# Kernel optimization log

Hardware: AMD Instinct MI355X
Metric: run time of the kernel (lower is better)

## Reference

```python
import jax, jax.numpy as jnp
import numpy as np

B, N, H, BIN, E = 16, 100, 300, 11, 20000


def setup_inputs() -> dict:
    key = jax.random.key(0)
    k1, k2, k3, k4, k5 = jax.random.split(key, 5)
    local_feats = jax.random.normal(k1, (B, N, H), dtype=jnp.float32)
    binary_feats = jax.random.normal(k2, (B, N, N, BIN), dtype=jnp.float32)
    sparse_idx = jax.random.randint(k3, (E, 3), 0, B).astype(jnp.int64)
    W1 = jax.random.normal(k4, (H + BIN, H), dtype=jnp.float32) * 0.02
    b1 = jnp.zeros((H,), dtype=jnp.float32)
    W2 = jax.random.normal(k5, (H, 1), dtype=jnp.float32) * 0.02
    b2 = jnp.zeros((1,), dtype=jnp.float32)
    return {"local_feats": local_feats, "binary_feats": binary_feats,
            "sparse_idx": sparse_idx, "W1": W1, "b1": b1, "W2": W2, "b2": b2}


def reference(local_feats, binary_feats, sparse_idx, W1, b1, W2, b2):
    # local_pair[b,i,j] = local_feats[b,j] + local_feats[b,i]  -> [B,N,N,H]
    local_pair = local_feats[:, None, :, :] + local_feats[:, :, None, :]
    all_feats = jnp.concatenate([local_pair, binary_feats], axis=-1)  # [B,N,N,H+BIN]
    att = jax.nn.relu(jnp.einsum('bijk,kh->bijh', all_feats, W1) + b1)  # [B,N,N,H]
    score = jax.nn.sigmoid(jnp.einsum('bijh,ho->bijo', att, W2) + b2)   # [B,N,N,1]
    # weighted sum over dim j (torch dim=2 of [B,1,N,H]*[B,N,N,1])
    global_feats = jnp.sum(local_feats[:, None, :, :] * score, axis=2)  # [B,N,H]
    bb, ii, jj = sparse_idx[:, 0], sparse_idx[:, 1], sparse_idx[:, 2]
    global_pair = global_feats[bb, ii] + global_feats[bb, jj]  # [E,H]
    local_pair_g = local_pair[bb, ii, jj]                      # [E,H]
    return (local_pair_g, global_pair)
```

## Files before the change

### kernel.cpp

```cpp
#include <hip/hip_runtime.h>

#define BB 16
#define NN 100
#define HH 300
#define EE 20000

typedef __bf16 bf16x8 __attribute__((ext_vector_type(8)));
typedef float f32x4 __attribute__((ext_vector_type(4)));

__device__ __forceinline__ unsigned short f2bf_u(float v) {
  const unsigned u = __builtin_bit_cast(unsigned, v);
  return (unsigned short)((u + 0x7FFFu + ((u >> 16) & 1u)) >> 16);
}
__device__ __forceinline__ __bf16 f2bf(float v) {
  unsigned short s = f2bf_u(v);
  return __builtin_bit_cast(__bf16, s);
}

#define OFF_GF 0
#define OFF_U 307200

__global__ __launch_bounds__(256) void k_projD(
    const float* __restrict__ X, const float* __restrict__ W1,
    const float* __restrict__ b1, const int* __restrict__ sp,
    float* __restrict__ out, float* __restrict__ U) {
  const int bid = (int)blockIdx.x;
  const int tid = (int)threadIdx.x;

  if (bid < 475) {
    const int wave = tid >> 6;
    const int lane = tid & 63;
    const int tile = bid * 4 + wave;
    const int mt = tile / 19;
    const int nt = tile - mt * 19;
    const int r0 = mt * 16;
    const int n0 = nt * 16;
    const int l15 = lane & 15;
    const int lk = (lane >> 4) * 8;

    bf16x8 xa[10];
    {
      const float* __restrict__ xr = X + (size_t)(r0 + l15) * 300;
#pragma unroll
      for (int kc = 0; kc < 10; ++kc) {
        const int k0 = lk + kc * 32;
        if (k0 + 7 < 300) {
          const float4 a = *reinterpret_cast<const float4*>(xr + k0);
          const float4 c = *reinterpret_cast<const float4*>(xr + k0 + 4);
          xa[kc][0] = f2bf(a.x); xa[kc][1] = f2bf(a.y);
          xa[kc][2] = f2bf(a.z); xa[kc][3] = f2bf(a.w);
          xa[kc][4] = f2bf(c.x); xa[kc][5] = f2bf(c.y);
          xa[kc][6] = f2bf(c.z); xa[kc][7] = f2bf(c.w);
        } else {
#pragma unroll
          for (int t = 0; t < 8; ++t) {
            const int k = k0 + t;
            xa[kc][t] = f2bf((k < 300) ? xr[k] : 0.f);
          }
        }
      }
    }
    bf16x8 wb[10];
    {
      const int col = n0 + l15;
      const bool cok = (col < 300);
#pragma unroll
      for (int kc = 0; kc < 10; ++kc) {
#pragma unroll
        for (int t = 0; t < 8; ++t) {
          const int k = lk + kc * 32 + t;
          const float v = (cok && k < 300) ? W1[(size_t)k * 300 + col] : 0.f;
          wb[kc][t] = f2bf(v);
        }
      }
    }

    f32x4 acc = {0.f, 0.f, 0.f, 0.f};
#pragma unroll
    for (int kc = 0; kc < 10; ++kc)
      acc = __builtin_amdgcn_mfma_f32_16x16x32_bf16(xa[kc], wb[kc], acc, 0, 0, 0);

    const int h = n0 + l15;
    if (h < 300) {
      const float hb = 0.5f * b1[h];
      const int rbase = r0 + (lane >> 4) * 4;
#pragma unroll
      for (int reg = 0; reg < 4; ++reg)
        U[(size_t)(rbase + reg) * 300 + h] = acc[reg] + hb;
    }
  } else {
    const float4* __restrict__ X4 = (const float4*)X;
    float4* __restrict__ out0 = (float4*)out;
    const int nb = (int)gridDim.x - 475;
    for (int idx = (bid - 475) * 256 + tid; idx < EE * 75; idx += nb * 256) {
      const int e = idx / 75;
      const int c = idx - e * 75;
      const int b = sp[e * 3 + 0];
      const int ii = sp[e * 3 + 1];
      const int jj = sp[e * 3 + 2];
      const float4 xi = X4[(b * 100 + ii) * 75 + c];
      const float4 xj = X4[(b * 100 + jj) * 75 + c];
      out0[idx] =
          make_float4(xi.x + xj.x, xi.y + xj.y, xi.z + xj.z, xi.w + xj.w);
    }
  }
}

__global__ __launch_bounds__(1024) void k_scoreGF3(
    const float* __restrict__ X, const float* __restrict__ U,
    const float* __restrict__ W1, const float* __restrict__ W2,
    const float* __restrict__ b2, const float* __restrict__ Bin,
    float* __restrict__ gf) {
  __shared__ float s_bin[1100];
  __shared__ float s_part[7][2][16];
  __shared__ float s_score[100];
  __shared__ float s_gpart[4][300];
  __shared__ __align__(16) unsigned short s_w1bt[304 * 40];

  const int bi = (int)blockIdx.x;
  const int b = bi >> 4;
  const int i = bi & 15;
  const int tid = (int)threadIdx.x;
  const int wv = tid >> 6;
  const int jt = wv >> 1;
  const int nth = wv & 1;
  const int lane = tid & 63;
  const int l15 = lane & 15;
  const int lk = (lane >> 4) * 8;

  for (int t = tid; t < 1100; t += 1024)
    s_bin[t] = Bin[(size_t)(b * 100 + i) * 1100 + t];
  for (int e = tid; e < 304 * 40; e += 1024) {
    const int row = e / 40;
    const int k = e - row * 40;
    float v = 0.f;
    if (k < 11 && row < 300) v = W1[(size_t)(300 + k) * 300 + row];
    s_w1bt[e] = f2bf_u(v);
  }
  __syncthreads();

  if (jt < 7) {
    bf16x8 af;
    const int jrl = jt * 16 + l15;
    const int jr_cl = (jrl < 100) ? jrl : 99;
#pragma unroll
    for (int t = 0; t < 8; ++t) {
      const int k = lk + t;
      af[t] = (k < 11) ? f2bf(s_bin[jr_cl * 11 + k]) : f2bf(0.f);
    }

    const int jbase = jt * 16 + (lane >> 4) * 4;
    int jrow[4];
#pragma unroll
    for (int reg = 0; reg < 4; ++reg)
      jrow[reg] = (jbase + reg < 100) ? (jbase + reg) : 99;

    const float* __restrict__ Ui = U + (size_t)(b * 100 + i) * 300;
    float jacc[4] = {0.f, 0.f, 0.f, 0.f};

    auto step = [&](int nt) {
      const bf16x8 bf = *reinterpret_cast<const bf16x8*>(
          &s_w1bt[(nt * 16 + l15) * 40 + lk]);
      const int h = nt * 16 + l15;
      const int hc = (h < 300) ? h : 299;
      const float ui = Ui[hc];
      const float w2v = (h < 300) ? W2[h] : 0.f;
      f32x4 cin;
#pragma unroll
      for (int reg = 0; reg < 4; ++reg)
        cin[reg] = ui + U[(size_t)(b * 100 + jrow[reg]) * 300 + hc];
      const f32x4 d =
          __builtin_amdgcn_mfma_f32_16x16x32_bf16(af, bf, cin, 0, 0, 0);
#pragma unroll
      for (int reg = 0; reg < 4; ++reg)
        jacc[reg] = fmaf(fmaxf(d[reg], 0.f), w2v, jacc[reg]);
    };
    if (nth == 0) {
#pragma unroll
      for (int t = 0; t < 10; ++t) step(t);
    } else {
#pragma unroll
      for (int t = 0; t < 9; ++t) step(10 + t);
    }

#pragma unroll
    for (int reg = 0; reg < 4; ++reg) {
      float p = jacc[reg];
#pragma unroll
      for (int m = 8; m >= 1; m >>= 1) p += __shfl_xor(p, m, 64);
      if (l15 == 0) s_part[jt][nth][(lane >> 4) * 4 + reg] = p;
    }
  }
  __syncthreads();

  if (tid < 100) {
    const float p = s_part[tid >> 4][0][tid & 15] +
                    s_part[tid >> 4][1][tid & 15] + b2[0];
    s_score[tid] = 1.f / (1.f + __expf(-p));
  }
  __syncthreads();

  for (int item = tid; item < 1200; item += 1024) {
    const int jq = item / 300;
    const int col = item - jq * 300;
    const float* __restrict__ Xr = X + (size_t)(b * 100 + jq * 25) * 300 + col;
    float g0 = 0.f, g1 = 0.f, g2 = 0.f, g3 = 0.f, g4 = 0.f;
#pragma unroll
    for (int jl = 0; jl < 25; jl += 5) {
      g0 = fmaf(Xr[(jl + 0) * 300], s_score[jq * 25 + jl + 0], g0);
      g1 = fmaf(Xr[(jl + 1) * 300], s_score[jq * 25 + jl + 1], g1);
      g2 = fmaf(Xr[(jl + 2) * 300], s_score[jq * 25 + jl + 2], g2);
      g3 = fmaf(Xr[(jl + 3) * 300], s_score[jq * 25 + jl + 3], g3);
      g4 = fmaf(Xr[(jl + 4) * 300], s_score[jq * 25 + jl + 4], g4);
    }
    s_gpart[jq][col] = ((g0 + g1) + (g2 + g3)) + g4;
  }
  __syncthreads();

  for (int col = tid; col < 300; col += 1024) {
    gf[bi * 300 + col] = (s_gpart[0][col] + s_gpart[1][col]) +
                         (s_gpart[2][col] + s_gpart[3][col]);
  }
}

__global__ __launch_bounds__(256) void k_out1(const int* __restrict__ sp,
                                              const float* __restrict__ gf,
                                              float* __restrict__ out) {
  const float4* __restrict__ G4 = (const float4*)gf;
  float4* __restrict__ out1 = (float4*)out + EE * 75;

  for (int idx = (int)blockIdx.x * 256 + (int)threadIdx.x; idx < EE * 75;
       idx += (int)gridDim.x * 256) {
    const int e = idx / 75;
    const int c = idx - e * 75;
    const int b = sp[e * 3 + 0];
    const int ii = sp[e * 3 + 1];
    const int jj = sp[e * 3 + 2];
    const float4 g1 = G4[(b * 16 + ii) * 75 + c];
    const float4 g2 = G4[(b * 16 + jj) * 75 + c];
    out1[idx] =
        make_float4(g1.x + g2.x, g1.y + g2.y, g1.z + g2.z, g1.w + g2.w);
  }
}

extern "C" void kernel_launch(void* const* d_in, const int* in_sizes, int n_in,
                              void* d_out, int out_size, void* d_ws,
                              size_t ws_size, hipStream_t stream) {
  const float* X   = (const float*)d_in[0];
  const float* Bin = (const float*)d_in[1];
  const int*   sp  = (const int*)d_in[2];
  const float* W1  = (const float*)d_in[3];
  const float* b1  = (const float*)d_in[4];
  const float* W2  = (const float*)d_in[5];
  const float* b2  = (const float*)d_in[6];
  float* out = (float*)d_out;

  char* wsb = (char*)d_ws;
  float* gf = (float*)(wsb + OFF_GF);
  float* U = (float*)(wsb + OFF_U);

  k_projD<<<1524, 256, 0, stream>>>(X, W1, b1, sp, out, U);
  k_scoreGF3<<<256, 1024, 0, stream>>>(X, U, W1, W2, b2, Bin, gf);
  k_out1<<<2048, 256, 0, stream>>>(sp, gf, out);
}
```

Measured before the change: 40.86 us.

## Precompute transposed bf16 W1 in workspace via separate prep kernel

Adds a prep kernel that converts W1 into a transposed, padded bf16 layout and builds a tiled bf16 layout of the binary-feature rows of W1. The projection kernel then loads B fragments as contiguous 16-byte vectors instead of doing 80 strided scalar loads and conversions per lane. The score kernel reads the prebuilt binary weight fragments from global memory instead of rebuilding a shared-memory copy in every block. This adds one kernel launch and a serial dependency in exchange for removing redundant conversion and uncoalesced weight loads.

```diff
diff --git a/kernel.cpp b/kernel.cpp
--- a/kernel.cpp
+++ b/kernel.cpp
@@ -18,10 +18,32 @@
 }
 
 #define OFF_GF 0
-#define OFF_U 307200
-
-__global__ __launch_bounds__(256) void k_projD(
-    const float* __restrict__ X, const float* __restrict__ W1,
+#define OFF_W1T 307200
+#define OFF_W1BT 501760
+#define OFF_U 521216
+
+__global__ __launch_bounds__(256) void k_prepW(const float* __restrict__ W1,
+                                               unsigned short* __restrict__ W1T,
+                                               unsigned short* __restrict__ W1BT) {
+  const int gtid = (int)blockIdx.x * 256 + (int)threadIdx.x;
+  const int gs = (int)gridDim.x * 256;
+  for (int e = gtid; e < 304 * 320; e += gs) {
+    const int j = e / 320, k = e - j * 320;
+    W1T[e] = f2bf_u((k < 300 && j < 300) ? W1[k * 300 + j] : 0.f);
+  }
+  for (int e = gtid; e < 19 * 512; e += gs) {
+    const int nt = e / 512;
+    const int r = (e & 511) >> 5;
+    const int k = e & 31;
+    const int h = nt * 16 + r;
+    float v = 0.f;
+    if (k < 11 && h < 300) v = W1[(300 + k) * 300 + h];
+    W1BT[e] = f2bf_u(v);
+  }
+}
+
+__global__ __launch_bounds__(256) void k_projX(
+    const float* __restrict__ X, const unsigned short* __restrict__ W1T,
     const float* __restrict__ b1, const int* __restrict__ sp,
     float* __restrict__ out, float* __restrict__ U) {
   const int bid = (int)blockIdx.x;
@@ -60,25 +82,14 @@
         }
       }
     }
-    bf16x8 wb[10];
-    {
-      const int col = n0 + l15;
-      const bool cok = (col < 300);
-#pragma unroll
-      for (int kc = 0; kc < 10; ++kc) {
-#pragma unroll
-        for (int t = 0; t < 8; ++t) {
-          const int k = lk + kc * 32 + t;
-          const float v = (cok && k < 300) ? W1[(size_t)k * 300 + col] : 0.f;
-          wb[kc][t] = f2bf(v);
-        }
-      }
-    }
 
     f32x4 acc = {0.f, 0.f, 0.f, 0.f};
-#pragma unroll
-    for (int kc = 0; kc < 10; ++kc)
-      acc = __builtin_amdgcn_mfma_f32_16x16x32_bf16(xa[kc], wb[kc], acc, 0, 0, 0);
+    const unsigned short* bp = W1T + (size_t)(n0 + l15) * 320 + lk;
+#pragma unroll
+    for (int kc = 0; kc < 10; ++kc) {
+      const bf16x8 bv = *reinterpret_cast<const bf16x8*>(bp + kc * 32);
+      acc = __builtin_amdgcn_mfma_f32_16x16x32_bf16(xa[kc], bv, acc, 0, 0, 0);
+    }
 
     const int h = n0 + l15;
     if (h < 300) {
@@ -106,16 +117,15 @@
   }
 }
 
-__global__ __launch_bounds__(1024) void k_scoreGF3(
+__global__ __launch_bounds__(1024) void k_scoreGF2(
     const float* __restrict__ X, const float* __restrict__ U,
-    const float* __restrict__ W1, const float* __restrict__ W2,
-    const float* __restrict__ b2, const float* __restrict__ Bin,
+    const float* __restrict__ W2, const float* __restrict__ b2,
+    const float* __restrict__ Bin, const unsigned short* __restrict__ W1BT,
     float* __restrict__ gf) {
   __shared__ float s_bin[1100];
   __shared__ float s_part[7][2][16];
   __shared__ float s_score[100];
   __shared__ float s_gpart[4][300];
-  __shared__ __align__(16) unsigned short s_w1bt[304 * 40];
 
   const int bi = (int)blockIdx.x;
   const int b = bi >> 4;
@@ -130,13 +140,6 @@
 
   for (int t = tid; t < 1100; t += 1024)
     s_bin[t] = Bin[(size_t)(b * 100 + i) * 1100 + t];
-  for (int e = tid; e < 304 * 40; e += 1024) {
-    const int row = e / 40;
-    const int k = e - row * 40;
-    float v = 0.f;
-    if (k < 11 && row < 300) v = W1[(size_t)(300 + k) * 300 + row];
-    s_w1bt[e] = f2bf_u(v);
-  }
   __syncthreads();
 
   if (jt < 7) {
@@ -159,8 +162,8 @@
     float jacc[4] = {0.f, 0.f, 0.f, 0.f};
 
     auto step = [&](int nt) {
-      const bf16x8 bf = *reinterpret_cast<const bf16x8*>(
-          &s_w1bt[(nt * 16 + l15) * 40 + lk]);
+      const bf16x8 bf =
+          *reinterpret_cast<const bf16x8*>(W1BT + (nt * 16 + l15) * 32 + lk);
       const int h = nt * 16 + l15;
       const int hc = (h < 300) ? h : 299;
       const float ui = Ui[hc];
@@ -257,9 +260,12 @@
 
   char* wsb = (char*)d_ws;
   float* gf = (float*)(wsb + OFF_GF);
+  unsigned short* W1T = (unsigned short*)(wsb + OFF_W1T);
+  unsigned short* W1BT = (unsigned short*)(wsb + OFF_W1BT);
   float* U = (float*)(wsb + OFF_U);
 
-  k_projD<<<1524, 256, 0, stream>>>(X, W1, b1, sp, out, U);
-  k_scoreGF3<<<256, 1024, 0, stream>>>(X, U, W1, W2, b2, Bin, gf);
+  k_prepW<<<424, 256, 0, stream>>>(W1, W1T, W1BT);
+  k_projX<<<1524, 256, 0, stream>>>(X, W1T, b1, sp, out, U);
+  k_scoreGF2<<<256, 1024, 0, stream>>>(X, U, W2, b2, Bin, W1BT, gf);
   k_out1<<<2048, 256, 0, stream>>>(sp, gf, out);
 }
```

After: 39.10 us. -4.3%, faster.

## Stage W1 tile and per-batch U rows in shared memory

Applied to the files above, without the earlier changes.

The projection kernel now stages a transposed bf16 slice of W1 (64 columns) in LDS once per block. Each block computes two M-tiles, so waves no longer each issue strided scalar global loads of W1. The score kernel copies the whole 100x300 U slice for its batch into padded LDS with coalesced loads, replacing the scattered per-lane global U gathers inside the MFMA loop. The trade-offs: the score kernel now uses nearly all of the CU's LDS, the transposed W1 writes may hit bank conflicts, and there are fewer GEMM blocks.

```diff
diff --git a/kernel.cpp b/kernel.cpp
--- a/kernel.cpp
+++ b/kernel.cpp
@@ -20,79 +20,87 @@
 #define OFF_GF 0
 #define OFF_U 307200
 
-__global__ __launch_bounds__(256) void k_projD(
+__global__ __launch_bounds__(256) void k_projW(
     const float* __restrict__ X, const float* __restrict__ W1,
     const float* __restrict__ b1, const int* __restrict__ sp,
     float* __restrict__ out, float* __restrict__ U) {
+  __shared__ __align__(16) unsigned short Ws[64][328];
+
   const int bid = (int)blockIdx.x;
   const int tid = (int)threadIdx.x;
 
-  if (bid < 475) {
+  if (bid < 250) {
+    const int ntg = bid / 50;
+    const int mtp = bid - ntg * 50;
+    const int c0 = ntg * 64;
+
+    for (int e = tid; e < 300 * 64; e += 256) {
+      const int k = e >> 6, c = e & 63;
+      const float v = (c0 + c < 300) ? W1[(size_t)k * 300 + c0 + c] : 0.f;
+      Ws[c][k] = f2bf_u(v);
+    }
+    for (int e = tid; e < 64 * 28; e += 256)
+      Ws[e / 28][300 + e % 28] = 0;
+    __syncthreads();
+
     const int wave = tid >> 6;
     const int lane = tid & 63;
-    const int tile = bid * 4 + wave;
-    const int mt = tile / 19;
-    const int nt = tile - mt * 19;
-    const int r0 = mt * 16;
-    const int n0 = nt * 16;
     const int l15 = lane & 15;
     const int lk = (lane >> 4) * 8;
-
-    bf16x8 xa[10];
-    {
-      const float* __restrict__ xr = X + (size_t)(r0 + l15) * 300;
-#pragma unroll
-      for (int kc = 0; kc < 10; ++kc) {
-        const int k0 = lk + kc * 32;
-        if (k0 + 7 < 300) {
-          const float4 a = *reinterpret_cast<const float4*>(xr + k0);
-          const float4 c = *reinterpret_cast<const float4*>(xr + k0 + 4);
-          xa[kc][0] = f2bf(a.x); xa[kc][1] = f2bf(a.y);
-          xa[kc][2] = f2bf(a.z); xa[kc][3] = f2bf(a.w);
-          xa[kc][4] = f2bf(c.x); xa[kc][5] = f2bf(c.y);
-          xa[kc][6] = f2bf(c.z); xa[kc][7] = f2bf(c.w);
-        } else {
-#pragma unroll
-          for (int t = 0; t < 8; ++t) {
-            const int k = k0 + t;
-            xa[kc][t] = f2bf((k < 300) ? xr[k] : 0.f);
+    const int nt = ntg * 4 + wave;
+
+    if (nt < 19) {
+#pragma unroll
+      for (int m = 0; m < 2; ++m) {
+        const int mt = mtp * 2 + m;
+        const int r0 = mt * 16;
+
+        bf16x8 xa[10];
+        {
+          const float* __restrict__ xr = X + (size_t)(r0 + l15) * 300;
+#pragma unroll
+          for (int kc = 0; kc < 10; ++kc) {
+            const int k0 = lk + kc * 32;
+            if (k0 + 7 < 300) {
+              const float4 a = *reinterpret_cast<const float4*>(xr + k0);
+              const float4 c = *reinterpret_cast<const float4*>(xr + k0 + 4);
+              xa[kc][0] = f2bf(a.x); xa[kc][1] = f2bf(a.y);
+              xa[kc][2] = f2bf(a.z); xa[kc][3] = f2bf(a.w);
+              xa[kc][4] = f2bf(c.x); xa[kc][5] = f2bf(c.y);
+              xa[kc][6] = f2bf(c.z); xa[kc][7] = f2bf(c.w);
+            } else {
+#pragma unroll
+              for (int t = 0; t < 8; ++t) {
+                const int k = k0 + t;
+                xa[kc][t] = f2bf((k < 300) ? xr[k] : 0.f);
+              }
+            }
           }
         }
-      }
-    }
-    bf16x8 wb[10];
-    {
-      const int col = n0 + l15;
-      const bool cok = (col < 300);
-#pragma unroll
-      for (int kc = 0; kc < 10; ++kc) {
-#pragma unroll
-        for (int t = 0; t < 8; ++t) {
-          const int k = lk + kc * 32 + t;
-          const float v = (cok && k < 300) ? W1[(size_t)k * 300 + col] : 0.f;
-          wb[kc][t] = f2bf(v);
+
+        f32x4 acc = {0.f, 0.f, 0.f, 0.f};
+#pragma unroll
+        for (int kc = 0; kc < 10; ++kc) {
+          const bf16x8 bv = *reinterpret_cast<const bf16x8*>(
+              &Ws[wave * 16 + l15][lk + kc * 32]);
+          acc = __builtin_amdgcn_mfma_f32_16x16x32_bf16(xa[kc], bv, acc, 0, 0, 0);
+        }
+
+        const int h = nt * 16 + l15;
+        if (h < 300) {
+          const float hb = 0.5f * b1[h];
+          const int rbase = r0 + (lane >> 4) * 4;
+#pragma unroll
+          for (int reg = 0; reg < 4; ++reg)
+            U[(size_t)(rbase + reg) * 300 + h] = acc[reg] + hb;
         }
       }
-    }
-
-    f32x4 acc = {0.f, 0.f, 0.f, 0.f};
-#pragma unroll
-    for (int kc = 0; kc < 10; ++kc)
-      acc = __builtin_amdgcn_mfma_f32_16x16x32_bf16(xa[kc], wb[kc], acc, 0, 0, 0);
-
-    const int h = n0 + l15;
-    if (h < 300) {
-      const float hb = 0.5f * b1[h];
-      const int rbase = r0 + (lane >> 4) * 4;
-#pragma unroll
-      for (int reg = 0; reg < 4; ++reg)
-        U[(size_t)(rbase + reg) * 300 + h] = acc[reg] + hb;
     }
   } else {
     const float4* __restrict__ X4 = (const float4*)X;
     float4* __restrict__ out0 = (float4*)out;
-    const int nb = (int)gridDim.x - 475;
-    for (int idx = (bid - 475) * 256 + tid; idx < EE * 75; idx += nb * 256) {
+    const int nb = (int)gridDim.x - 250;
+    for (int idx = (bid - 250) * 256 + tid; idx < EE * 75; idx += nb * 256) {
       const int e = idx / 75;
       const int c = idx - e * 75;
       const int b = sp[e * 3 + 0];
@@ -106,16 +114,18 @@
   }
 }
 
-__global__ __launch_bounds__(1024) void k_scoreGF3(
+#define USTR 308
+__global__ __launch_bounds__(1024) void k_scoreGF3L(
     const float* __restrict__ X, const float* __restrict__ U,
     const float* __restrict__ W1, const float* __restrict__ W2,
     const float* __restrict__ b2, const float* __restrict__ Bin,
     float* __restrict__ gf) {
+  __shared__ float s_U[100 * USTR];
+  __shared__ __align__(16) unsigned short s_w1bt[304 * 40];
   __shared__ float s_bin[1100];
   __shared__ float s_part[7][2][16];
   __shared__ float s_score[100];
   __shared__ float s_gpart[4][300];
-  __shared__ __align__(16) unsigned short s_w1bt[304 * 40];
 
   const int bi = (int)blockIdx.x;
   const int b = bi >> 4;
@@ -128,8 +138,16 @@
   const int l15 = lane & 15;
   const int lk = (lane >> 4) * 8;
 
-  for (int t = tid; t < 1100; t += 1024)
-    s_bin[t] = Bin[(size_t)(b * 100 + i) * 1100 + t];
+  {
+    const float* __restrict__ Ub = U + (size_t)b * 100 * 300;
+    for (int e = tid; e < 100 * 300; e += 1024) {
+      const int row = e / 300;
+      const int col = e - row * 300;
+      s_U[row * USTR + col] = Ub[e];
+    }
+    for (int e = tid; e < 100 * 8; e += 1024)
+      s_U[(e >> 3) * USTR + 300 + (e & 7)] = 0.f;
+  }
   for (int e = tid; e < 304 * 40; e += 1024) {
     const int row = e / 40;
     const int k = e - row * 40;
@@ -137,6 +155,8 @@
     if (k < 11 && row < 300) v = W1[(size_t)(300 + k) * 300 + row];
     s_w1bt[e] = f2bf_u(v);
   }
+  for (int t = tid; t < 1100; t += 1024)
+    s_bin[t] = Bin[(size_t)(b * 100 + i) * 1100 + t];
   __syncthreads();
 
   if (jt < 7) {
@@ -155,20 +175,18 @@
     for (int reg = 0; reg < 4; ++reg)
       jrow[reg] = (jbase + reg < 100) ? (jbase + reg) : 99;
 
-    const float* __restrict__ Ui = U + (size_t)(b * 100 + i) * 300;
     float jacc[4] = {0.f, 0.f, 0.f, 0.f};
 
     auto step = [&](int nt) {
       const bf16x8 bf = *reinterpret_cast<const bf16x8*>(
           &s_w1bt[(nt * 16 + l15) * 40 + lk]);
       const int h = nt * 16 + l15;
-      const int hc = (h < 300) ? h : 299;
-      const float ui = Ui[hc];
+      const float ui = s_U[i * USTR + h];
       const float w2v = (h < 300) ? W2[h] : 0.f;
       f32x4 cin;
 #pragma unroll
       for (int reg = 0; reg < 4; ++reg)
-        cin[reg] = ui + U[(size_t)(b * 100 + jrow[reg]) * 300 + hc];
+        cin[reg] = ui + s_U[jrow[reg] * USTR + h];
       const f32x4 d =
           __builtin_amdgcn_mfma_f32_16x16x32_bf16(af, bf, cin, 0, 0, 0);
 #pragma unroll
@@ -259,7 +277,7 @@
   float* gf = (float*)(wsb + OFF_GF);
   float* U = (float*)(wsb + OFF_U);
 
-  k_projD<<<1524, 256, 0, stream>>>(X, W1, b1, sp, out, U);
-  k_scoreGF3<<<256, 1024, 0, stream>>>(X, U, W1, W2, b2, Bin, gf);
+  k_projW<<<1524, 256, 0, stream>>>(X, W1, b1, sp, out, U);
+  k_scoreGF3L<<<256, 1024, 0, stream>>>(X, U, W1, W2, b2, Bin, gf);
   k_out1<<<2048, 256, 0, stream>>>(sp, gf, out);
 }
```

Measured after the change: 52.30 us. +28.0%, slower.
